# Kernel tuning notes

Measured on AMD Instinct MI355X. Metric: run time of the kernel, lower is better.

Reference implementation:

```python
import jax, jax.numpy as jnp
import numpy as np

MD = 4  # max displacement -> (2*MD+1)**2 = 81 output channels

def setup_inputs() -> dict:
    key = jax.random.key(0)
    k1, k2 = jax.random.split(key)
    B, C, H, W = 4, 128, 128, 256
    t1 = jax.random.normal(k1, (B, C, H, W), dtype=jnp.float32)
    t2 = jax.random.normal(k2, (B, C, H, W), dtype=jnp.float32)
    return {"t1": t1, "t2": t2}

def reference(t1, t2):
    # PWC-Net correlation: for each displacement (dy,dx) in [-MD,MD]^2,
    # corr[b, d, y, x] = mean_c t1[b,c,y,x] * t2[b,c,y+dy,x+dx]
    B, C, H, W = t1.shape
    t2p = jnp.pad(t2, ((0, 0), (0, 0), (MD, MD), (MD, MD)))
    outs = []
    for dy in range(2 * MD + 1):
        for dx in range(2 * MD + 1):
            shifted = t2p[:, :, dy:dy + H, dx:dx + W]  # (B,C,H,W)
            outs.append(jnp.mean(t1 * shifted, axis=1))  # (B,H,W)
    return jnp.stack(outs, axis=1)  # (B, 81, H, W)
```

## Files before the change

### kernel.cpp

```cpp
#include <hip/hip_runtime.h>

#define MD   4
#define B_   4
#define C_   128
#define H_   128
#define W_   256
#define ND   9
#define NW   9
#define XPT  8

typedef float float4v __attribute__((ext_vector_type(4)));

__global__ __launch_bounds__(NW * 64, 3)
void corr_kernel(const float* __restrict__ t1,
                 const float* __restrict__ t2,
                 float* __restrict__ out) {
    const int tid  = threadIdx.x;
    const int lane = tid & 63;
    const int w    = tid >> 6;
    const int bid  = blockIdx.x;
    const int swz  = (bid & 7) * 32 + (bid >> 3);
    const int yp   = swz & 63;
    const int b    = swz >> 6;
    const int y0   = yp * 2;
    const int half = lane >> 5;
    const int lx   = lane & 31;
    const int x0   = lx * XPT;
    const int yrow = y0 + half;
    const int yy   = yrow + w - MD;
    const bool live = (0 <= yy) && (yy < H_);
    const int  yc  = yy < 0 ? 0 : (yy > H_ - 1 ? H_ - 1 : yy);
    const float sc = live ? (1.0f / (float)C_) : 0.0f;
    const bool lm  = (lx == 0);
    const bool rm  = (lx == 31);
    const int offL = lm ? 0 : -4;
    const int offR = rm ? 0 :  8;

    float acc[ND][XPT];
    #pragma unroll
    for (int dx = 0; dx < ND; ++dx)
        #pragma unroll
        for (int j = 0; j < XPT; ++j) acc[dx][j] = 0.0f;

    const float* p1 = t1 + (((size_t)(b * C_)) * H_ + yrow) * W_ + x0;
    const float* p2 = t2 + (((size_t)(b * C_)) * H_ + yc  ) * W_ + x0;
    const size_t chstr = (size_t)H_ * W_;

    #pragma unroll 2
    for (int c = 0; c < C_; ++c) {
        const float* pc1 = p1 + (size_t)c * chstr;
        const float* pc2 = p2 + (size_t)c * chstr;
        const float4v a0 = *(const float4v*)(pc1);
        const float4v a1 = *(const float4v*)(pc1 + 4);

        float4v wl = *(const float4v*)(pc2 + offL);
        const float4v v0 = *(const float4v*)(pc2);
        const float4v v1 = *(const float4v*)(pc2 + 4);
        float4v wr = *(const float4v*)(pc2 + offR);
        #pragma unroll
        for (int q = 0; q < 4; ++q) {
            wl[q] = lm ? 0.0f : wl[q];
            wr[q] = rm ? 0.0f : wr[q];
        }

        float win[XPT + 2 * MD];
        #pragma unroll
        for (int q = 0; q < 4; ++q) {
            win[q]      = wl[q];
            win[4 + q]  = v0[q];
            win[8 + q]  = v1[q];
            win[12 + q] = wr[q];
        }

        #pragma unroll
        for (int dx = 0; dx < ND; ++dx)
            #pragma unroll
            for (int j = 0; j < XPT; ++j) {
                const float aj = (j < 4) ? a0[j] : a1[j - 4];
                acc[dx][j] = fmaf(aj, win[dx + j], acc[dx][j]);
            }
    }

    #pragma unroll
    for (int dx = 0; dx < ND; ++dx) {
        float4v o0, o1;
        #pragma unroll
        for (int j = 0; j < 4; ++j) {
            o0[j] = acc[dx][j]     * sc;
            o1[j] = acc[dx][4 + j] * sc;
        }
        const size_t oidx =
            (((size_t)(b * ND * ND) + w * ND + dx) * H_ + yrow) * W_ + x0;
        *(float4v*)&out[oidx]     = o0;
        *(float4v*)&out[oidx + 4] = o1;
    }
}

extern "C" void kernel_launch(void* const* d_in, const int* in_sizes, int n_in,
                              void* d_out, int out_size, void* d_ws, size_t ws_size,
                              hipStream_t stream) {
    const float* t1 = (const float*)d_in[0];
    const float* t2 = (const float*)d_in[1];
    float* out      = (float*)d_out;
    corr_kernel<<<dim3(B_ * H_ / 2), NW * 64, 0, stream>>>(t1, t2, out);
}
```

Baseline: 76.40 us.

## Stage t2 rows in shared memory via async global_load_lds double buffering

Each block now loads the 10 t2 rows it needs per channel pair into LDS with global_load_lds, double-buffered across channel phases. The nine waves then read their shifted windows from swizzled LDS instead of each re-fetching overlapping rows from global memory. This is meant to cut redundant global/L2 traffic for t2 and to overlap the next phase's loads with compute. In exchange it adds a block-wide barrier per two channels and about 40KB of LDS per block, which may limit occupancy.

```diff
diff --git a/kernel.cpp b/kernel.cpp
--- a/kernel.cpp
+++ b/kernel.cpp
@@ -8,6 +8,9 @@
 #define ND   9
 #define NW   9
 #define XPT  8
+#define CHK  2
+#define NPH  (C_ / CHK)
+#define NROW 10
 
 typedef float float4v __attribute__((ext_vector_type(4)));
 
@@ -15,6 +18,8 @@
 void corr_kernel(const float* __restrict__ t1,
                  const float* __restrict__ t2,
                  float* __restrict__ out) {
+    __shared__ __align__(16) float t2s[2][CHK][NROW][W_];
+
     const int tid  = threadIdx.x;
     const int lane = tid & 63;
     const int w    = tid >> 6;
@@ -29,12 +34,18 @@
     const int yrow = y0 + half;
     const int yy   = yrow + w - MD;
     const bool live = (0 <= yy) && (yy < H_);
-    const int  yc  = yy < 0 ? 0 : (yy > H_ - 1 ? H_ - 1 : yy);
     const float sc = live ? (1.0f / (float)C_) : 0.0f;
     const bool lm  = (lx == 0);
     const bool rm  = (lx == 31);
-    const int offL = lm ? 0 : -4;
-    const int offR = rm ? 0 :  8;
+    const int r_lds = w + half;
+
+    const int j0 = lm ? 0  : 2 * lx - 1;
+    const int j1 = 2 * lx;
+    const int j2 = 2 * lx + 1;
+    const int j3 = rm ? 63 : 2 * lx + 2;
+#define SWZB(j) ((((j) ^ (((j) >> 3) & 7)) << 4))
+    const int o0 = SWZB(j0), o1 = SWZB(j1), o2 = SWZB(j2), o3 = SWZB(j3);
+    const int jsrc = lane ^ ((lane >> 3) & 7);
 
     float acc[ND][XPT];
     #pragma unroll
@@ -43,42 +54,72 @@
         for (int j = 0; j < XPT; ++j) acc[dx][j] = 0.0f;
 
     const float* p1 = t1 + (((size_t)(b * C_)) * H_ + yrow) * W_ + x0;
-    const float* p2 = t2 + (((size_t)(b * C_)) * H_ + yc  ) * W_ + x0;
     const size_t chstr = (size_t)H_ * W_;
 
-    #pragma unroll 2
-    for (int c = 0; c < C_; ++c) {
-        const float* pc1 = p1 + (size_t)c * chstr;
-        const float* pc2 = p2 + (size_t)c * chstr;
-        const float4v a0 = *(const float4v*)(pc1);
-        const float4v a1 = *(const float4v*)(pc1 + 4);
+    auto STAGE = [&](int buf, int ph) {
+        const int c0 = ph * CHK;
+        #pragma unroll
+        for (int k = 0; k < 3; ++k) {
+            const int s = w + k * NW;
+            if (s < CHK * NROW) {
+                const int ch2 = s / NROW;
+                const int r   = s % NROW;
+                int grow = y0 - MD + r;
+                grow = grow < 0 ? 0 : (grow > H_ - 1 ? H_ - 1 : grow);
+                const float* src =
+                    t2 + (((size_t)(b * C_ + c0 + ch2)) * H_ + grow) * W_ + jsrc * 4;
+                __builtin_amdgcn_global_load_lds(
+                    (const __attribute__((address_space(1))) unsigned int*)src,
+                    (__attribute__((address_space(3))) unsigned int*)&t2s[buf][ch2][r][0],
+                    16, 0, 0);
+            }
+        }
+    };
 
-        float4v wl = *(const float4v*)(pc2 + offL);
-        const float4v v0 = *(const float4v*)(pc2);
-        const float4v v1 = *(const float4v*)(pc2 + 4);
-        float4v wr = *(const float4v*)(pc2 + offR);
+    STAGE(0, 0);
+    __syncthreads();
+
+    for (int ph = 0; ph < NPH; ++ph) {
+        const int buf = ph & 1;
+        if (ph + 1 < NPH) STAGE(buf ^ 1, ph + 1);
+
+        const int c0 = ph * CHK;
         #pragma unroll
-        for (int q = 0; q < 4; ++q) {
-            wl[q] = lm ? 0.0f : wl[q];
-            wr[q] = rm ? 0.0f : wr[q];
+        for (int ch = 0; ch < CHK; ++ch) {
+            const float* pc1 = p1 + (size_t)(c0 + ch) * chstr;
+            const float4v a0 = *(const float4v*)(pc1);
+            const float4v a1 = *(const float4v*)(pc1 + 4);
+
+            const char* row =
+                (const char*)&t2s[buf][ch][0][0] + r_lds * (W_ * 4);
+            float4v wl = *(const float4v*)(row + o0);
+            const float4v v0 = *(const float4v*)(row + o1);
+            const float4v v1 = *(const float4v*)(row + o2);
+            float4v wr = *(const float4v*)(row + o3);
+            #pragma unroll
+            for (int q = 0; q < 4; ++q) {
+                wl[q] = lm ? 0.0f : wl[q];
+                wr[q] = rm ? 0.0f : wr[q];
+            }
+
+            float win[XPT + 2 * MD];
+            #pragma unroll
+            for (int q = 0; q < 4; ++q) {
+                win[q]      = wl[q];
+                win[4 + q]  = v0[q];
+                win[8 + q]  = v1[q];
+                win[12 + q] = wr[q];
+            }
+
+            #pragma unroll
+            for (int dx = 0; dx < ND; ++dx)
+                #pragma unroll
+                for (int j = 0; j < XPT; ++j) {
+                    const float aj = (j < 4) ? a0[j] : a1[j - 4];
+                    acc[dx][j] = fmaf(aj, win[dx + j], acc[dx][j]);
+                }
         }
-
-        float win[XPT + 2 * MD];
-        #pragma unroll
-        for (int q = 0; q < 4; ++q) {
-            win[q]      = wl[q];
-            win[4 + q]  = v0[q];
-            win[8 + q]  = v1[q];
-            win[12 + q] = wr[q];
-        }
-
-        #pragma unroll
-        for (int dx = 0; dx < ND; ++dx)
-            #pragma unroll
-            for (int j = 0; j < XPT; ++j) {
-                const float aj = (j < 4) ? a0[j] : a1[j - 4];
-                acc[dx][j] = fmaf(aj, win[dx + j], acc[dx][j]);
-            }
+        __syncthreads();
     }
 
     #pragma unroll
```

After: 75.57 us. No clear change (-1.1%).

## Stage t1/t2 rows into double-buffered LDS via global_load_lds

Applied to the files above, without the earlier changes.

Each block now stages 4 channels at a time of its 2 t1 rows and the 10 t2 rows it needs into a double-buffered shared-memory tile, using direct global-to-LDS loads with a permuted lane layout. All 9 waves then read their shifted windows from LDS instead of each issuing its own overlapping global loads. The next channel group is prefetched while the current one is computed. The aim is to remove the redundant global and L1 traffic for t2 rows shared across waves and to hide load latency. In exchange the kernel uses about 98KB of LDS, which limits occupancy to one block per CU, and adds a block barrier per channel group.

```diff
diff --git a/kernel.cpp b/kernel.cpp
--- a/kernel.cpp
+++ b/kernel.cpp
@@ -8,13 +8,18 @@
 #define ND   9
 #define NW   9
 #define XPT  8
+#define CC   4
+#define NPH  (C_ / CC)
+#define NRW  12
 
 typedef float float4v __attribute__((ext_vector_type(4)));
 
-__global__ __launch_bounds__(NW * 64, 3)
+__global__ __launch_bounds__(NW * 64, 2)
 void corr_kernel(const float* __restrict__ t1,
                  const float* __restrict__ t2,
                  float* __restrict__ out) {
+    __shared__ __align__(16) float lds[2][CC][NRW][W_];
+
     const int tid  = threadIdx.x;
     const int lane = tid & 63;
     const int w    = tid >> 6;
@@ -29,12 +34,12 @@
     const int yrow = y0 + half;
     const int yy   = yrow + w - MD;
     const bool live = (0 <= yy) && (yy < H_);
-    const int  yc  = yy < 0 ? 0 : (yy > H_ - 1 ? H_ - 1 : yy);
     const float sc = live ? (1.0f / (float)C_) : 0.0f;
     const bool lm  = (lx == 0);
     const bool rm  = (lx == 31);
-    const int offL = lm ? 0 : -4;
-    const int offR = rm ? 0 :  8;
+    const int lxm  = lm ? 0  : lx - 1;
+    const int lxp  = rm ? lx : lx + 1;
+    const int jsrc = ((lane & 31) << 1) | (lane >> 5);
 
     float acc[ND][XPT];
     #pragma unroll
@@ -42,43 +47,72 @@
         #pragma unroll
         for (int j = 0; j < XPT; ++j) acc[dx][j] = 0.0f;
 
-    const float* p1 = t1 + (((size_t)(b * C_)) * H_ + yrow) * W_ + x0;
-    const float* p2 = t2 + (((size_t)(b * C_)) * H_ + yc  ) * W_ + x0;
-    const size_t chstr = (size_t)H_ * W_;
+    auto STAGE = [&](int buf, int ph) {
+        const int c0 = ph * CC;
+        #pragma unroll
+        for (int k = 0; k < 6; ++k) {
+            const int s = w + k * NW;
+            if (s < CC * NRW) {
+                const int ch = s / NRW;
+                const int r  = s % NRW;
+                const float* src;
+                if (r < 2) {
+                    src = t1 + (((size_t)(b * C_ + c0 + ch)) * H_ + (y0 + r)) * W_
+                            + jsrc * 4;
+                } else {
+                    int gr = y0 + r - 6;
+                    gr = gr < 0 ? 0 : (gr > H_ - 1 ? H_ - 1 : gr);
+                    src = t2 + (((size_t)(b * C_ + c0 + ch)) * H_ + gr) * W_
+                            + jsrc * 4;
+                }
+                __builtin_amdgcn_global_load_lds(
+                    (const __attribute__((address_space(1))) unsigned int*)src,
+                    (__attribute__((address_space(3))) unsigned int*)&lds[buf][ch][r][0],
+                    16, 0, 0);
+            }
+        }
+    };
 
-    #pragma unroll 2
-    for (int c = 0; c < C_; ++c) {
-        const float* pc1 = p1 + (size_t)c * chstr;
-        const float* pc2 = p2 + (size_t)c * chstr;
-        const float4v a0 = *(const float4v*)(pc1);
-        const float4v a1 = *(const float4v*)(pc1 + 4);
+    STAGE(0, 0);
+    __syncthreads();
 
-        float4v wl = *(const float4v*)(pc2 + offL);
-        const float4v v0 = *(const float4v*)(pc2);
-        const float4v v1 = *(const float4v*)(pc2 + 4);
-        float4v wr = *(const float4v*)(pc2 + offR);
-        #pragma unroll
-        for (int q = 0; q < 4; ++q) {
-            wl[q] = lm ? 0.0f : wl[q];
-            wr[q] = rm ? 0.0f : wr[q];
+    for (int t = 0; t < NPH; ++t) {
+        const int buf = t & 1;
+        if (t + 1 < NPH) STAGE(buf ^ 1, t + 1);
+
+        for (int ch = 0; ch < CC; ++ch) {
+            const float* s1 = &lds[buf][ch][half][0];
+            const float* s2 = &lds[buf][ch][2 + w + half][0];
+            const float4v a0 = *(const float4v*)(s1 + lx * 4);
+            const float4v a1 = *(const float4v*)(s1 + 128 + lx * 4);
+            const float4v v0 = *(const float4v*)(s2 + lx * 4);
+            const float4v v1 = *(const float4v*)(s2 + 128 + lx * 4);
+            float4v wl = *(const float4v*)(s2 + 128 + lxm * 4);
+            float4v wr = *(const float4v*)(s2 + lxp * 4);
+            #pragma unroll
+            for (int q = 0; q < 4; ++q) {
+                wl[q] = lm ? 0.0f : wl[q];
+                wr[q] = rm ? 0.0f : wr[q];
+            }
+
+            float win[XPT + 2 * MD];
+            #pragma unroll
+            for (int q = 0; q < 4; ++q) {
+                win[q]      = wl[q];
+                win[4 + q]  = v0[q];
+                win[8 + q]  = v1[q];
+                win[12 + q] = wr[q];
+            }
+
+            #pragma unroll
+            for (int dx = 0; dx < ND; ++dx)
+                #pragma unroll
+                for (int j = 0; j < XPT; ++j) {
+                    const float aj = (j < 4) ? a0[j] : a1[j - 4];
+                    acc[dx][j] = fmaf(aj, win[dx + j], acc[dx][j]);
+                }
         }
-
-        float win[XPT + 2 * MD];
-        #pragma unroll
-        for (int q = 0; q < 4; ++q) {
-            win[q]      = wl[q];
-            win[4 + q]  = v0[q];
-            win[8 + q]  = v1[q];
-            win[12 + q] = wr[q];
-        }
-
-        #pragma unroll
-        for (int dx = 0; dx < ND; ++dx)
-            #pragma unroll
-            for (int j = 0; j < XPT; ++j) {
-                const float aj = (j < 4) ? a0[j] : a1[j - 4];
-                acc[dx][j] = fmaf(aj, win[dx + j], acc[dx][j]);
-            }
+        __syncthreads();
     }
 
     #pragma unroll
```

Measured after the change: 112.2 us. +46.9%, slower.

## Convert inputs to channel-packed bf16 and compute correlation with MFMA

Applied to the files above, without the earlier changes.

Adds a pre-pass that converts t1 and t2 to bf16 in a channel-inner packed layout in the workspace. A new kernel then computes each displacement row as 16x16x32 bf16 MFMA products between t1 pixels and a window of t2 pixels, and extracts the diagonal bands through shared memory. The aim is to move the scalar FMA-bound channel reduction onto matrix cores. The cost is an extra launch, extra workspace traffic, bf16 precision loss, and wasted MFMA work on the unused off-diagonal products. The old kernel is kept as a fallback for when the workspace is too small.

```diff
diff --git a/kernel.cpp b/kernel.cpp
--- a/kernel.cpp
+++ b/kernel.cpp
@@ -6,15 +6,134 @@
 #define H_   128
 #define W_   256
 #define ND   9
-#define NW   9
-#define XPT  8
-
-typedef float float4v __attribute__((ext_vector_type(4)));
-
-__global__ __launch_bounds__(NW * 64, 3)
-void corr_kernel(const float* __restrict__ t1,
-                 const float* __restrict__ t2,
-                 float* __restrict__ out) {
+
+typedef float  float4v __attribute__((ext_vector_type(4)));
+typedef float  f32x4   __attribute__((ext_vector_type(4)));
+typedef short  bf16x8  __attribute__((ext_vector_type(8)));
+typedef unsigned int u32;
+typedef u32    u32x4   __attribute__((ext_vector_type(4)));
+
+static __device__ __forceinline__ unsigned short f2bf(float f) {
+    u32 u = __float_as_uint(f);
+    u32 r = (u + 0x7fffu + ((u >> 16) & 1u)) >> 16;
+    return (unsigned short)r;
+}
+
+__global__ __launch_bounds__(256)
+void convert_kernel(const float* __restrict__ t1,
+                    const float* __restrict__ t2,
+                    unsigned short* __restrict__ ws) {
+    const int bid = blockIdx.x;
+    const int kc  = bid & 3;
+    const int y   = (bid >> 2) & (H_ - 1);
+    const int b   = (bid >> 9) & 3;
+    const int tn  = bid >> 11;
+    const float* src = tn ? t2 : t1;
+    unsigned short* dst = ws + (size_t)tn * ((size_t)B_ * H_ * 4 * W_ * 32)
+                             + ((((size_t)(b * H_ + y)) * 4 + kc) * W_) * 32;
+    const int x = threadIdx.x;
+
+    u32 pk[16];
+    #pragma unroll
+    for (int i = 0; i < 16; ++i) {
+        const float f0 = src[((size_t)(b * C_ + kc * 32 + 2 * i    ) * H_ + y) * W_ + x];
+        const float f1 = src[((size_t)(b * C_ + kc * 32 + 2 * i + 1) * H_ + y) * W_ + x];
+        pk[i] = (u32)f2bf(f0) | ((u32)f2bf(f1) << 16);
+    }
+    u32x4* po = (u32x4*)(dst + (size_t)x * 32);
+    #pragma unroll
+    for (int q = 0; q < 4; ++q) {
+        u32x4 v;
+        #pragma unroll
+        for (int j = 0; j < 4; ++j) v[j] = pk[q * 4 + j];
+        po[q] = v;
+    }
+}
+
+__global__ __launch_bounds__(512, 2)
+void corr_mfma_kernel(const unsigned short* __restrict__ ws,
+                      float* __restrict__ out) {
+    __shared__ float scr[8][2 * 16 * 33];
+
+    const int tid = threadIdx.x;
+    const int l   = tid & 63;
+    const int w   = tid >> 6;
+    const int bid = blockIdx.x;
+    const int swz = (bid & 7) * 64 + (bid >> 3);
+    const int y   = swz & (H_ - 1);
+    const int b   = swz >> 7;
+    const int ln  = l & 15;
+    const int kg  = l >> 4;
+    const unsigned short* t1w = ws;
+    const unsigned short* t2w = ws + (size_t)B_ * H_ * 4 * W_ * 32;
+    const float scale = 1.0f / (float)C_;
+    const bf16x8 z8 = (bf16x8)(short)0;
+
+    for (int t = 0; t < 2; ++t) {
+        const int X0 = (2 * w + t) * 16;
+
+        f32x4 acc0[ND], acc1[ND];
+        #pragma unroll
+        for (int r = 0; r < ND; ++r) { acc0[r] = (f32x4)0.0f; acc1[r] = (f32x4)0.0f; }
+
+        int col0 = X0 - 8 + ln;
+        int col1 = X0 + 8 + ln;
+        const bool ob0 = col0 < 0;
+        const bool ob1 = col1 > W_ - 1;
+        col0 = ob0 ? 0 : col0;
+        col1 = ob1 ? W_ - 1 : col1;
+
+        #pragma unroll
+        for (int kc = 0; kc < 4; ++kc) {
+            const unsigned short* a_base =
+                t1w + ((((size_t)(b * H_ + y)) * 4 + kc) * W_) * 32;
+            const bf16x8 a = *(const bf16x8*)(a_base + (size_t)(X0 + ln) * 32 + kg * 8);
+            #pragma unroll
+            for (int r = 0; r < ND; ++r) {
+                const int row = y + r - MD;
+                if (0 <= row && row < H_) {
+                    const unsigned short* b_base =
+                        t2w + ((((size_t)(b * H_ + row)) * 4 + kc) * W_) * 32;
+                    bf16x8 b0 = *(const bf16x8*)(b_base + (size_t)col0 * 32 + kg * 8);
+                    bf16x8 b1 = *(const bf16x8*)(b_base + (size_t)col1 * 32 + kg * 8);
+                    b0 = ob0 ? z8 : b0;
+                    b1 = ob1 ? z8 : b1;
+                    acc0[r] = __builtin_amdgcn_mfma_f32_16x16x32_bf16(a, b0, acc0[r], 0, 0, 0);
+                    acc1[r] = __builtin_amdgcn_mfma_f32_16x16x32_bf16(a, b1, acc1[r], 0, 0, 0);
+                }
+            }
+        }
+
+        float* sw = scr[w];
+        #pragma unroll
+        for (int r = 0; r < ND; ++r) {
+            const int row = y + r - MD;
+            const bool liv = (0 <= row && row < H_);
+            #pragma unroll
+            for (int i = 0; i < 4; ++i) {
+                sw[(kg * 4 + i) * 33 + ln]       = acc0[r][i];
+                sw[528 + (kg * 4 + i) * 33 + ln] = acc1[r][i];
+            }
+            #pragma unroll
+            for (int i = 0; i < 3; ++i) {
+                const int dx = i * 4 + kg;
+                if (dx < ND) {
+                    const int m  = ln;
+                    const int md = m + dx;
+                    const int idx = (md < 12) ? (m * 33 + md + 4)
+                                              : (528 + m * 33 + md - 12);
+                    const float v = liv ? sw[idx] * scale : 0.0f;
+                    out[((((size_t)b * 81) + r * ND + dx) * H_ + y) * W_ + X0 + m] = v;
+                }
+            }
+        }
+    }
+}
+
+__global__ __launch_bounds__(9 * 64, 3)
+void corr_fallback(const float* __restrict__ t1,
+                   const float* __restrict__ t2,
+                   float* __restrict__ out) {
     const int tid  = threadIdx.x;
     const int lane = tid & 63;
     const int w    = tid >> 6;
@@ -25,7 +144,7 @@
     const int y0   = yp * 2;
     const int half = lane >> 5;
     const int lx   = lane & 31;
-    const int x0   = lx * XPT;
+    const int x0   = lx * 8;
     const int yrow = y0 + half;
     const int yy   = yrow + w - MD;
     const bool live = (0 <= yy) && (yy < H_);
@@ -36,11 +155,11 @@
     const int offL = lm ? 0 : -4;
     const int offR = rm ? 0 :  8;
 
-    float acc[ND][XPT];
+    float acc[ND][8];
     #pragma unroll
     for (int dx = 0; dx < ND; ++dx)
         #pragma unroll
-        for (int j = 0; j < XPT; ++j) acc[dx][j] = 0.0f;
+        for (int j = 0; j < 8; ++j) acc[dx][j] = 0.0f;
 
     const float* p1 = t1 + (((size_t)(b * C_)) * H_ + yrow) * W_ + x0;
     const float* p2 = t2 + (((size_t)(b * C_)) * H_ + yc  ) * W_ + x0;
@@ -52,7 +171,6 @@
         const float* pc2 = p2 + (size_t)c * chstr;
         const float4v a0 = *(const float4v*)(pc1);
         const float4v a1 = *(const float4v*)(pc1 + 4);
-
         float4v wl = *(const float4v*)(pc2 + offL);
         const float4v v0 = *(const float4v*)(pc2);
         const float4v v1 = *(const float4v*)(pc2 + 4);
@@ -62,20 +180,16 @@
             wl[q] = lm ? 0.0f : wl[q];
             wr[q] = rm ? 0.0f : wr[q];
         }
-
-        float win[XPT + 2 * MD];
+        float win[16];
         #pragma unroll
         for (int q = 0; q < 4; ++q) {
-            win[q]      = wl[q];
-            win[4 + q]  = v0[q];
-            win[8 + q]  = v1[q];
-            win[12 + q] = wr[q];
-        }
-
+            win[q] = wl[q]; win[4 + q] = v0[q];
+            win[8 + q] = v1[q]; win[12 + q] = wr[q];
+        }
         #pragma unroll
         for (int dx = 0; dx < ND; ++dx)
             #pragma unroll
-            for (int j = 0; j < XPT; ++j) {
+            for (int j = 0; j < 8; ++j) {
                 const float aj = (j < 4) ? a0[j] : a1[j - 4];
                 acc[dx][j] = fmaf(aj, win[dx + j], acc[dx][j]);
             }
@@ -86,7 +200,7 @@
         float4v o0, o1;
         #pragma unroll
         for (int j = 0; j < 4; ++j) {
-            o0[j] = acc[dx][j]     * sc;
+            o0[j] = acc[dx][j] * sc;
             o1[j] = acc[dx][4 + j] * sc;
         }
         const size_t oidx =
@@ -102,5 +216,12 @@
     const float* t1 = (const float*)d_in[0];
     const float* t2 = (const float*)d_in[1];
     float* out      = (float*)d_out;
-    corr_kernel<<<dim3(B_ * H_ / 2), NW * 64, 0, stream>>>(t1, t2, out);
-}
+    const size_t need = (size_t)2 * B_ * H_ * 4 * W_ * 32 * sizeof(unsigned short);
+    if (ws_size >= need) {
+        unsigned short* ws = (unsigned short*)d_ws;
+        convert_kernel<<<dim3(2 * B_ * H_ * 4), 256, 0, stream>>>(t1, t2, ws);
+        corr_mfma_kernel<<<dim3(B_ * H_), 512, 0, stream>>>(ws, out);
+    } else {
+        corr_fallback<<<dim3(B_ * H_ / 2), 9 * 64, 0, stream>>>(t1, t2, out);
+    }
+}
```

Measured after the change: 94.51 us. +23.7%, slower.
